# Optimization experiments

Measured on AMD Instinct MI355X. Metric: run time of the kernel, lower is better.

Reference implementation:

```python
import jax, jax.numpy as jnp
import numpy as np
from jax import lax

DT = 0.1


def setup_inputs() -> dict:
    key = jax.random.key(0)
    k1, k2, k3, k4 = jax.random.split(key, 4)
    Bsz, L, D, N, O = 32, 2048, 256, 64, 256
    x = jax.random.normal(k1, (Bsz, L, D), dtype=jnp.float32)
    # Shift A by 3*I so Re(eig(A)) > 0 -> bilinear-discretized A_tilde is stable
    A = jax.random.uniform(k2, (N, N), dtype=jnp.float32) + 3.0 * jnp.eye(N, dtype=jnp.float32)
    B = jax.random.uniform(k3, (N, D), dtype=jnp.float32)
    C = jax.random.uniform(k4, (O, N), dtype=jnp.float32)
    return {"x": x, "A": A, "B": B, "C": C}


def _s4_forward(x, A, B, C):
    N = A.shape[0]
    I = jnp.eye(N, dtype=A.dtype)
    # Bilinear discretization (as written in the torch source)
    tmp_inv = jnp.linalg.inv(I + A * (DT / 2))
    A_tilde = tmp_inv @ (I - A * (DT / 2))          # [N, N]
    B_tilde = (tmp_inv @ B) * DT                    # [N, D]

    L = x.shape[1]

    # K[i] = C @ A_tilde^i @ B_tilde; carry M = A_tilde^i @ B_tilde
    def step(M, _):
        return A_tilde @ M, C @ M                    # emit [O, D]

    _, K = lax.scan(step, B_tilde, None, length=L)   # K: [L, O, D]

    n = 2 * L - 1  # length after torch's F.pad(x, (0,0,0,L-1))
    x_fft = jnp.fft.rfft(x, n=n, axis=1)             # [B, F, D] complex
    K_fft = jnp.fft.rfft(K, n=n, axis=0)             # [F, O, D] complex
    y_fft = jnp.einsum('bfi,foi->bfo', x_fft, K_fft)
    y = jnp.fft.irfft(y_fft, n=n, axis=1)[:, :L]     # [B, L, O]
    return y


def reference(x, A, B, C):
    return _s4_forward(x, A, B, C)
```

## Files before the change

### kernel.cpp

```cpp
#include <hip/hip_runtime.h>

#define B_SZ   32
#define LEN    2048
#define DIM    256
#define NST    64
#define OUTD   256
#define CHUNK  32
#define NCHUNK (LEN / CHUNK)
#define ROWS   (B_SZ * LEN)
#define NCID   (B_SZ * NCHUNK)

#define OFF_AT   0
#define OFF_P32  4096
#define OFF_MINV 8192
#define OFF_CP   12288
#define OFF_S    28672
#define OFF_INST 159744
#define OFF_V    290816
#define WS_FLOATS (OFF_V + (size_t)ROWS * 64)

__device__ __forceinline__ void gload16(const float* gp, float* lds_base,
                                        int lane_off_f) {
#if __has_builtin(__builtin_amdgcn_global_load_lds)
  (void)lane_off_f;
  __builtin_amdgcn_global_load_lds(
      (const __attribute__((address_space(1))) unsigned int*)gp,
      (__attribute__((address_space(3))) unsigned int*)lds_base, 16, 0, 0);
#else
  float4 tmp = *(const float4*)gp;
  *(float4*)(lds_base + lane_off_f) = tmp;
#endif
}

__device__ __forceinline__ void mm64(float* dst, const float* a, const float* b,
                                     int t) {
  const int r0 = 4 * (t >> 4), c0 = 4 * (t & 15);
  float acc[4][4] = {};
  for (int k = 0; k < 64; ++k) {
    float4 bv = *(const float4*)(b + k * 68 + c0);
#pragma unroll
    for (int i = 0; i < 4; ++i) {
      float av = a[(r0 + i) * 68 + k];
      acc[i][0] = fmaf(av, bv.x, acc[i][0]);
      acc[i][1] = fmaf(av, bv.y, acc[i][1]);
      acc[i][2] = fmaf(av, bv.z, acc[i][2]);
      acc[i][3] = fmaf(av, bv.w, acc[i][3]);
    }
  }
  __syncthreads();
#pragma unroll
  for (int i = 0; i < 4; ++i)
    *(float4*)(dst + (r0 + i) * 68 + c0) =
        make_float4(acc[i][0], acc[i][1], acc[i][2], acc[i][3]);
  __syncthreads();
}

__global__ __launch_bounds__(256) void k_fused0(const float* __restrict__ A,
                                                const float* __restrict__ Bm,
                                                const float* __restrict__ Cm,
                                                const float* __restrict__ x,
                                                float* __restrict__ ws) {
  __shared__ __align__(16) float sh[13056];
  const int t = threadIdx.x;

  if (blockIdx.x == 0) {
    float* Pa = sh;
    float* Pb = sh + 4352;
    float* Pc = sh + 8704;
    float* rbM = Pc;
    float* rbI = Pc + 128;
    float* cb  = Pc + 256;

    const int tc = t & 63;
    const int tr = t >> 6;
    float M[16], Iv[16];
#pragma unroll
    for (int i = 0; i < 16; ++i) {
      int r = 16 * tr + i;
      M[i] = 0.05f * A[r * 64 + tc] + (r == tc ? 1.0f : 0.0f);
      Iv[i] = (r == tc) ? 1.0f : 0.0f;
    }
    if (tr == 0) { rbM[tc] = M[0]; rbI[tc] = Iv[0]; }
    if (tc == 0)
      for (int i = 0; i < 16; ++i) cb[16 * tr + i] = M[i];
    __syncthreads();

#pragma unroll
    for (int k = 0; k < 64; ++k) {
      const int cur = (k & 1) * 64, nxt = ((k + 1) & 1) * 64;
      float rinv = 1.0f / rbM[cur + k];
      float rM = rbM[cur + tc] * rinv;
      float rI = rbI[cur + tc] * rinv;
#pragma unroll
      for (int i = 0; i < 16; ++i) {
        int r = 16 * tr + i;
        if (r == k) { M[i] = rM; Iv[i] = rI; }
        else {
          float f = cb[cur + r];
          M[i] = fmaf(-f, rM, M[i]);
          Iv[i] = fmaf(-f, rI, Iv[i]);
        }
      }
      if (k < 63) {
        if (tr == ((k + 1) >> 4)) {
          rbM[nxt + tc] = M[(k + 1) & 15];
          rbI[nxt + tc] = Iv[(k + 1) & 15];
        }
        if (tc == k + 1)
          for (int i = 0; i < 16; ++i) cb[nxt + 16 * tr + i] = M[i];
      }
      __syncthreads();
    }

#pragma unroll
    for (int i = 0; i < 16; ++i) {
      int r = 16 * tr + i;
      float at = 2.0f * Iv[i] - (r == tc ? 1.0f : 0.0f);
      ws[OFF_AT + r * 64 + tc] = at;
      ws[OFF_MINV + r * 64 + tc] = Iv[i];
      Pa[r * 68 + tc] = at;
      Pc[r * 68 + tc] = Iv[i];
    }
    __syncthreads();

    mm64(Pb, Pa, Pa, t);
    mm64(Pa, Pb, Pb, t);
    mm64(Pb, Pa, Pa, t);
    mm64(Pa, Pb, Pb, t);
    mm64(Pb, Pa, Pa, t);
#pragma unroll
    for (int i = 0; i < 16; ++i) {
      int r = 16 * tr + i;
      ws[OFF_P32 + r * 64 + tc] = Pb[r * 68 + tc];
    }

    {
      const float* Crow = Cm + (size_t)t * 64;
      float4 acc4[16];
      for (int q = 0; q < 16; ++q) acc4[q] = make_float4(0.f, 0.f, 0.f, 0.f);
      for (int k = 0; k < 64; k += 4) {
        float4 c4 = *(const float4*)(Crow + k);
        float ck[4] = {c4.x, c4.y, c4.z, c4.w};
#pragma unroll
        for (int kk = 0; kk < 4; ++kk) {
          const float* mrow = Pc + (k + kk) * 68;
          float cc = ck[kk];
#pragma unroll
          for (int q = 0; q < 16; ++q) {
            float4 mv = *(const float4*)(mrow + 4 * q);
            acc4[q].x = fmaf(cc, mv.x, acc4[q].x);
            acc4[q].y = fmaf(cc, mv.y, acc4[q].y);
            acc4[q].z = fmaf(cc, mv.z, acc4[q].z);
            acc4[q].w = fmaf(cc, mv.w, acc4[q].w);
          }
        }
      }
      float* cp = ws + OFF_CP + (size_t)t * 64;
      for (int q = 0; q < 16; ++q)
        *(float4*)(cp + 4 * q) =
            make_float4(0.1f * acc4[q].x, 0.1f * acc4[q].y, 0.1f * acc4[q].z,
                        0.1f * acc4[q].w);
    }
  } else {
    float* xsT = sh;
    float* bsT = sh + 4352;
    const int rowbase = ((int)blockIdx.x - 1) * 64;
    const int r0 = 4 * (t >> 4), m0 = 4 * (t & 15);
    float acc[4][4] = {};
    for (int db = 0; db < 4; ++db) {
      int d0 = db * 64;
      for (int i = 0; i < 4; ++i) {
        int e = 4 * (t + 256 * i);
        int rr = e >> 6, dd = e & 63;
        float4 xv = *(const float4*)(x + (size_t)(rowbase + rr) * 256 + d0 + dd);
        xsT[(dd + 0) * 68 + rr] = xv.x;
        xsT[(dd + 1) * 68 + rr] = xv.y;
        xsT[(dd + 2) * 68 + rr] = xv.z;
        xsT[(dd + 3) * 68 + rr] = xv.w;
        float4 bv = *(const float4*)(Bm + (size_t)rr * 256 + d0 + dd);
        bsT[(dd + 0) * 68 + rr] = bv.x;
        bsT[(dd + 1) * 68 + rr] = bv.y;
        bsT[(dd + 2) * 68 + rr] = bv.z;
        bsT[(dd + 3) * 68 + rr] = bv.w;
      }
      __syncthreads();
      for (int k = 0; k < 64; ++k) {
        float4 av4 = *(const float4*)(xsT + k * 68 + r0);
        float4 bv4 = *(const float4*)(bsT + k * 68 + m0);
        float av[4] = {av4.x, av4.y, av4.z, av4.w};
        float bv[4] = {bv4.x, bv4.y, bv4.z, bv4.w};
        for (int i = 0; i < 4; ++i)
          for (int j = 0; j < 4; ++j) acc[i][j] = fmaf(av[i], bv[j], acc[i][j]);
      }
      __syncthreads();
    }
    float* v = ws + OFF_V;
    for (int i = 0; i < 4; ++i)
      *(float4*)(v + (size_t)(rowbase + r0 + i) * 64 + m0) =
          make_float4(acc[i][0], acc[i][1], acc[i][2], acc[i][3]);
  }
}

__global__ __launch_bounds__(256, 4) void k_chunk(float* __restrict__ ws,
                                                  int phase) {
  __shared__ __align__(16) float Hs[4 * CHUNK * 64];
  __shared__ __align__(16) float hb[4 * 64];
  const int t = threadIdx.x, w = t >> 6, lane = t & 63;
  const int cid = blockIdx.x * 4 + w;
  const int b = cid >> 6, c = cid & (NCHUNK - 1);
  const int r = lane;

  float a[64];
#pragma unroll
  for (int k4 = 0; k4 < 16; ++k4) {
    float4 v4 = *(const float4*)(ws + OFF_AT + r * 64 + 4 * k4);
    a[4 * k4 + 0] = v4.x; a[4 * k4 + 1] = v4.y;
    a[4 * k4 + 2] = v4.z; a[4 * k4 + 3] = v4.w;
  }

  float* Hw = Hs + w * (CHUNK * 64);
  const float* u = ws + OFF_V + (size_t)(b * LEN + c * CHUNK) * 64;
#pragma unroll
  for (int q = 0; q < 8; ++q)
    gload16(u + q * 256 + lane * 4, Hw + q * 256, lane * 4);

  float h0 = (phase == 3)
                 ? ws[OFF_INST + (size_t)(b * NCHUNK + c) * 64 + r]
                 : 0.0f;
  asm volatile("s_waitcnt vmcnt(0)" ::: "memory");
  float* hw = hb + w * 64;
  hw[r] = h0;
  asm volatile("" ::: "memory");

  float* hout = ws + OFF_V + (size_t)(b * LEN + c * CHUNK) * 64;
  float hlast = h0;
#pragma unroll 4
  for (int tt = 0; tt < CHUNK; ++tt) {
    float ac0 = 0.f, ac1 = 0.f, ac2 = 0.f, ac3 = 0.f;
#pragma unroll
    for (int k = 0; k < 64; k += 4) {
      float4 hv = *(const float4*)(hw + k);
      ac0 = fmaf(a[k + 0], hv.x, ac0);
      ac1 = fmaf(a[k + 1], hv.y, ac1);
      ac2 = fmaf(a[k + 2], hv.z, ac2);
      ac3 = fmaf(a[k + 3], hv.w, ac3);
    }
    float hn = ((ac0 + ac1) + (ac2 + ac3)) + Hw[tt * 64 + r];
    hw[r] = hn;
    if (phase == 3) hout[(size_t)tt * 64 + r] = hn;
    hlast = hn;
    asm volatile("" ::: "memory");
  }
  if (phase != 3) ws[OFF_S + (size_t)(b * NCHUNK + c) * 64 + r] = hlast;
}

__global__ __launch_bounds__(256) void k_carry(float* __restrict__ ws) {
  __shared__ __align__(16) float hbc[4][64];
  const int t = threadIdx.x, w = t >> 6, lane = t & 63;
  const int b = blockIdx.x * 4 + w;
  const int r = lane;
  float a[64];
#pragma unroll
  for (int k4 = 0; k4 < 16; ++k4) {
    float4 v4 = *(const float4*)(ws + OFF_P32 + r * 64 + 4 * k4);
    a[4 * k4 + 0] = v4.x; a[4 * k4 + 1] = v4.y;
    a[4 * k4 + 2] = v4.z; a[4 * k4 + 3] = v4.w;
  }
  const float* S = ws + OFF_S + (size_t)b * (NCHUNK * 64);
  float* INST = ws + OFF_INST + (size_t)b * (NCHUNK * 64);
  INST[r] = 0.0f;
  float* hw = hbc[w];
  hw[r] = 0.0f;
  float s_pre = S[r];
  asm volatile("" ::: "memory");
  for (int cc = 1; cc < NCHUNK; ++cc) {
    float s_nxt = (cc < NCHUNK - 1) ? S[(size_t)cc * 64 + r] : 0.0f;
    float ac0 = 0.f, ac1 = 0.f, ac2 = 0.f, ac3 = 0.f;
#pragma unroll
    for (int k = 0; k < 64; k += 4) {
      float4 hv = *(const float4*)(hw + k);
      ac0 = fmaf(a[k + 0], hv.x, ac0);
      ac1 = fmaf(a[k + 1], hv.y, ac1);
      ac2 = fmaf(a[k + 2], hv.z, ac2);
      ac3 = fmaf(a[k + 3], hv.w, ac3);
    }
    float hn = ((ac0 + ac1) + (ac2 + ac3)) + s_pre;
    hw[r] = hn;
    INST[(size_t)cc * 64 + r] = hn;
    s_pre = s_nxt;
    asm volatile("" ::: "memory");
  }
}

__global__ __launch_bounds__(256) void k_ygemm(const float* __restrict__ ws,
                                               float* __restrict__ y) {
  __shared__ __align__(16) float hs[64 * 68];
  __shared__ __align__(16) float cs[64 * 68];
  const int t = threadIdx.x;
  const int rowbase = blockIdx.x * 64;
  const int o0 = blockIdx.y * 64;
  const float* h = ws + OFF_V;
  const float* CP = ws + OFF_CP;
  for (int i = 0; i < 4; ++i) {
    int e = 4 * (t + 256 * i);
    int rr = e >> 6, nn = e & 63;
    *(float4*)(hs + rr * 68 + nn) =
        *(const float4*)(h + (size_t)rowbase * 64 + e);
    float4 cv = *(const float4*)(CP + (size_t)(o0 + rr) * 64 + nn);
    cs[(nn + 0) * 68 + rr] = cv.x;
    cs[(nn + 1) * 68 + rr] = cv.y;
    cs[(nn + 2) * 68 + rr] = cv.z;
    cs[(nn + 3) * 68 + rr] = cv.w;
  }
  __syncthreads();
  const int tr = t >> 4, tc = t & 15;
  const int r0 = tr * 4, c0 = tc * 4;
  float acc[4][4] = {};
  for (int k = 0; k < 64; ++k) {
    float4 cv4 = *(const float4*)(cs + k * 68 + c0);
    float cv[4] = {cv4.x, cv4.y, cv4.z, cv4.w};
    for (int i = 0; i < 4; ++i) {
      float hv = hs[(r0 + i) * 68 + k];
      for (int j = 0; j < 4; ++j) acc[i][j] = fmaf(hv, cv[j], acc[i][j]);
    }
  }
  for (int i = 0; i < 4; ++i)
    *(float4*)(y + (size_t)(rowbase + r0 + i) * 256 + o0 + c0) =
        make_float4(acc[i][0], acc[i][1], acc[i][2], acc[i][3]);
}

extern "C" void kernel_launch(void* const* d_in, const int* in_sizes, int n_in,
                              void* d_out, int out_size, void* d_ws,
                              size_t ws_size, hipStream_t stream) {
  const float* x = (const float*)d_in[0];
  const float* A = (const float*)d_in[1];
  const float* Bm = (const float*)d_in[2];
  const float* Cm = (const float*)d_in[3];
  float* y = (float*)d_out;
  float* ws = (float*)d_ws;
  if (ws_size < (size_t)WS_FLOATS * sizeof(float)) return;

  hipLaunchKernelGGL(k_fused0, dim3(1 + ROWS / 64), dim3(256), 0, stream, A,
                     Bm, Cm, x, ws);
  hipLaunchKernelGGL(k_chunk, dim3(NCID / 4), dim3(256), 0, stream, ws, 1);
  hipLaunchKernelGGL(k_carry, dim3(B_SZ / 4), dim3(256), 0, stream, ws);
  hipLaunchKernelGGL(k_chunk, dim3(NCID / 4), dim3(256), 0, stream, ws, 3);
  hipLaunchKernelGGL(k_ygemm, dim3(ROWS / 64, OUTD / 64), dim3(256), 0, stream,
                     ws, y);
}
```

Measured before the change: 250.2 us.

## Use split-bf16 MFMA for input and output projections, move P32/CP setup into chunk kernel

Rewrites the x·Bᵀ projection and the h·CPᵀ output GEMM to run on bf16 MFMA. Each fp32 operand is split into a high and a low bf16 part, and three MFMAs per tile (hi·hi, lo·hi, hi·lo) recover near-fp32 accuracy. Operands are staged in XOR-swizzled LDS via global_load_lds. The A_tilde^32 power and C·Minv precompute move out of the serial block 0 of k_fused0 into two extra blocks of the first k_chunk launch, shortening the critical path of the first kernel. The split-bf16 scheme trades some precision for matrix-core throughput, and the ygemm grid becomes one block per 64 rows covering all 256 outputs.

```diff
diff --git a/kernel.cpp b/kernel.cpp
--- a/kernel.cpp
+++ b/kernel.cpp
@@ -18,6 +18,10 @@
 #define OFF_INST 159744
 #define OFF_V    290816
 #define WS_FLOATS (OFF_V + (size_t)ROWS * 64)
+
+typedef __attribute__((ext_vector_type(8))) short bf16x8;
+typedef __attribute__((ext_vector_type(4))) float f32x4;
+union U4 { uint4 u; bf16x8 b; };
 
 __device__ __forceinline__ void gload16(const float* gp, float* lds_base,
                                         int lane_off_f) {
@@ -32,6 +36,29 @@
 #endif
 }
 
+__device__ __forceinline__ void split8(float4 a, float4 b, uint4& h, uint4& l) {
+  unsigned int ua0 = __float_as_uint(a.x), ua1 = __float_as_uint(a.y);
+  unsigned int ua2 = __float_as_uint(a.z), ua3 = __float_as_uint(a.w);
+  unsigned int ub0 = __float_as_uint(b.x), ub1 = __float_as_uint(b.y);
+  unsigned int ub2 = __float_as_uint(b.z), ub3 = __float_as_uint(b.w);
+  h.x = (ua0 >> 16) | (ua1 & 0xFFFF0000u);
+  h.y = (ua2 >> 16) | (ua3 & 0xFFFF0000u);
+  h.z = (ub0 >> 16) | (ub1 & 0xFFFF0000u);
+  h.w = (ub2 >> 16) | (ub3 & 0xFFFF0000u);
+  float l0 = a.x - __uint_as_float(ua0 & 0xFFFF0000u);
+  float l1 = a.y - __uint_as_float(ua1 & 0xFFFF0000u);
+  float l2 = a.z - __uint_as_float(ua2 & 0xFFFF0000u);
+  float l3 = a.w - __uint_as_float(ua3 & 0xFFFF0000u);
+  float l4 = b.x - __uint_as_float(ub0 & 0xFFFF0000u);
+  float l5 = b.y - __uint_as_float(ub1 & 0xFFFF0000u);
+  float l6 = b.z - __uint_as_float(ub2 & 0xFFFF0000u);
+  float l7 = b.w - __uint_as_float(ub3 & 0xFFFF0000u);
+  l.x = (__float_as_uint(l0) >> 16) | (__float_as_uint(l1) & 0xFFFF0000u);
+  l.y = (__float_as_uint(l2) >> 16) | (__float_as_uint(l3) & 0xFFFF0000u);
+  l.z = (__float_as_uint(l4) >> 16) | (__float_as_uint(l5) & 0xFFFF0000u);
+  l.w = (__float_as_uint(l6) >> 16) | (__float_as_uint(l7) & 0xFFFF0000u);
+}
+
 __device__ __forceinline__ void mm64(float* dst, const float* a, const float* b,
                                      int t) {
   const int r0 = 4 * (t >> 4), c0 = 4 * (t & 15);
@@ -57,20 +84,15 @@
 
 __global__ __launch_bounds__(256) void k_fused0(const float* __restrict__ A,
                                                 const float* __restrict__ Bm,
-                                                const float* __restrict__ Cm,
                                                 const float* __restrict__ x,
                                                 float* __restrict__ ws) {
-  __shared__ __align__(16) float sh[13056];
+  __shared__ __align__(16) float sh[16384];
   const int t = threadIdx.x;
 
   if (blockIdx.x == 0) {
-    float* Pa = sh;
-    float* Pb = sh + 4352;
-    float* Pc = sh + 8704;
-    float* rbM = Pc;
-    float* rbI = Pc + 128;
-    float* cb  = Pc + 256;
-
+    float* rbM = sh;
+    float* rbI = sh + 128;
+    float* cb  = sh + 256;
     const int tc = t & 63;
     const int tr = t >> 6;
     float M[16], Iv[16];
@@ -84,7 +106,6 @@
     if (tc == 0)
       for (int i = 0; i < 16; ++i) cb[16 * tr + i] = M[i];
     __syncthreads();
-
 #pragma unroll
     for (int k = 0; k < 64; ++k) {
       const int cur = (k & 1) * 64, nxt = ((k + 1) & 1) * 64;
@@ -111,101 +132,136 @@
       }
       __syncthreads();
     }
-
 #pragma unroll
     for (int i = 0; i < 16; ++i) {
       int r = 16 * tr + i;
-      float at = 2.0f * Iv[i] - (r == tc ? 1.0f : 0.0f);
-      ws[OFF_AT + r * 64 + tc] = at;
+      ws[OFF_AT + r * 64 + tc] = 2.0f * Iv[i] - (r == tc ? 1.0f : 0.0f);
       ws[OFF_MINV + r * 64 + tc] = Iv[i];
-      Pa[r * 68 + tc] = at;
-      Pc[r * 68 + tc] = Iv[i];
+    }
+  } else {
+    float* Bl = sh;
+    const int w = t >> 6, lane = t & 63;
+#pragma unroll
+    for (int c2 = 0; c2 < 16; ++c2) {
+      int n = 16 * w + c2;
+      const float* gp = Bm + (size_t)n * 256 + 4 * (lane ^ (n & 7));
+      gload16(gp, Bl + n * 256, lane * 4);
     }
     __syncthreads();
 
-    mm64(Pb, Pa, Pa, t);
-    mm64(Pa, Pb, Pb, t);
-    mm64(Pb, Pa, Pa, t);
-    mm64(Pa, Pb, Pb, t);
-    mm64(Pb, Pa, Pa, t);
-#pragma unroll
-    for (int i = 0; i < 16; ++i) {
-      int r = 16 * tr + i;
-      ws[OFF_P32 + r * 64 + tc] = Pb[r * 68 + tc];
-    }
-
-    {
-      const float* Crow = Cm + (size_t)t * 64;
-      float4 acc4[16];
-      for (int q = 0; q < 16; ++q) acc4[q] = make_float4(0.f, 0.f, 0.f, 0.f);
-      for (int k = 0; k < 64; k += 4) {
-        float4 c4 = *(const float4*)(Crow + k);
-        float ck[4] = {c4.x, c4.y, c4.z, c4.w};
-#pragma unroll
-        for (int kk = 0; kk < 4; ++kk) {
-          const float* mrow = Pc + (k + kk) * 68;
-          float cc = ck[kk];
-#pragma unroll
-          for (int q = 0; q < 16; ++q) {
-            float4 mv = *(const float4*)(mrow + 4 * q);
-            acc4[q].x = fmaf(cc, mv.x, acc4[q].x);
-            acc4[q].y = fmaf(cc, mv.y, acc4[q].y);
-            acc4[q].z = fmaf(cc, mv.z, acc4[q].z);
-            acc4[q].w = fmaf(cc, mv.w, acc4[q].w);
+    const int rowbase = ((int)blockIdx.x - 1) * 64 + 16 * w;
+    const int rr = lane & 15, kb = lane >> 4, key = lane & 7;
+    const float* xp = x + (size_t)(rowbase + rr) * 256 + 8 * kb;
+    f32x4 acc[4] = {{0.f,0.f,0.f,0.f},{0.f,0.f,0.f,0.f},
+                    {0.f,0.f,0.f,0.f},{0.f,0.f,0.f,0.f}};
+    float4 xc0 = *(const float4*)(xp);
+    float4 xc1 = *(const float4*)(xp + 4);
+#pragma unroll
+    for (int ki = 0; ki < 8; ++ki) {
+      float4 xn0, xn1;
+      if (ki < 7) {
+        xn0 = *(const float4*)(xp + 32 * (ki + 1));
+        xn1 = *(const float4*)(xp + 32 * (ki + 1) + 4);
+      }
+      U4 ah, al;
+      split8(xc0, xc1, ah.u, al.u);
+#pragma unroll
+      for (int nt = 0; nt < 4; ++nt) {
+        const float* brow = Bl + (nt * 16 + rr) * 256;
+        int U0 = 8 * ki + 2 * kb;
+        float4 b0 = *(const float4*)(brow + 4 * (U0 ^ key));
+        float4 b1 = *(const float4*)(brow + 4 * ((U0 + 1) ^ key));
+        U4 bh, bl2;
+        split8(b0, b1, bh.u, bl2.u);
+        acc[nt] = __builtin_amdgcn_mfma_f32_16x16x32_bf16(ah.b, bh.b, acc[nt], 0, 0, 0);
+        acc[nt] = __builtin_amdgcn_mfma_f32_16x16x32_bf16(al.b, bh.b, acc[nt], 0, 0, 0);
+        acc[nt] = __builtin_amdgcn_mfma_f32_16x16x32_bf16(ah.b, bl2.b, acc[nt], 0, 0, 0);
+      }
+      if (ki < 7) { xc0 = xn0; xc1 = xn1; }
+    }
+    float* v = ws + OFF_V;
+#pragma unroll
+    for (int nt = 0; nt < 4; ++nt)
+#pragma unroll
+      for (int j = 0; j < 4; ++j)
+        v[(size_t)(rowbase + 4 * kb + j) * 64 + nt * 16 + rr] = acc[nt][j];
+  }
+}
+
+__global__ __launch_bounds__(256, 4) void k_chunk(float* __restrict__ ws,
+                                                  const float* __restrict__ Cm,
+                                                  int phase) {
+  __shared__ __align__(16) float sh[8704];
+  float* Hs = sh;
+  float* hb = sh + 8192;
+  const int t = threadIdx.x, w = t >> 6, lane = t & 63;
+
+  if (blockIdx.x >= NCID / 4) {
+    if (phase != 1) return;
+    if (blockIdx.x == NCID / 4) {
+      float* Pa = sh;
+      float* Pb = sh + 4352;
+#pragma unroll
+      for (int i = 0; i < 4; ++i) {
+        int e = 4 * (t + 256 * i);
+        int r = e >> 6, c2 = e & 63;
+        *(float4*)(Pa + r * 68 + c2) = *(const float4*)(ws + OFF_AT + e);
+      }
+      __syncthreads();
+      mm64(Pb, Pa, Pa, t);
+      mm64(Pa, Pb, Pb, t);
+      mm64(Pb, Pa, Pa, t);
+      mm64(Pa, Pb, Pb, t);
+      mm64(Pb, Pa, Pa, t);
+#pragma unroll
+      for (int i = 0; i < 4; ++i) {
+        int e = 4 * (t + 256 * i);
+        int r = e >> 6, c2 = e & 63;
+        *(float4*)(ws + OFF_P32 + e) = *(const float4*)(Pb + r * 68 + c2);
+      }
+    } else {
+      float* Ms = sh;
+      float* Cs = sh + 4352;
+#pragma unroll
+      for (int i = 0; i < 4; ++i) {
+        int e = 4 * (t + 256 * i);
+        int kk = e >> 6, nn = e & 63;
+        *(float4*)(Ms + kk * 68 + nn) = *(const float4*)(ws + OFF_MINV + e);
+      }
+      __syncthreads();
+      const int r0 = 4 * (t >> 4), c0 = 4 * (t & 15);
+      for (int ob = 0; ob < 4; ++ob) {
+#pragma unroll
+        for (int i = 0; i < 4; ++i) {
+          int e = 4 * (t + 256 * i);
+          int orow = e >> 6, kk = e & 63;
+          *(float4*)(Cs + orow * 68 + kk) =
+              *(const float4*)(Cm + (size_t)(64 * ob + orow) * 64 + kk);
+        }
+        __syncthreads();
+        float acc[4][4] = {};
+        for (int k = 0; k < 64; ++k) {
+          float4 bv = *(const float4*)(Ms + k * 68 + c0);
+#pragma unroll
+          for (int i = 0; i < 4; ++i) {
+            float av = Cs[(r0 + i) * 68 + k];
+            acc[i][0] = fmaf(av, bv.x, acc[i][0]);
+            acc[i][1] = fmaf(av, bv.y, acc[i][1]);
+            acc[i][2] = fmaf(av, bv.z, acc[i][2]);
+            acc[i][3] = fmaf(av, bv.w, acc[i][3]);
           }
         }
-      }
-      float* cp = ws + OFF_CP + (size_t)t * 64;
-      for (int q = 0; q < 16; ++q)
-        *(float4*)(cp + 4 * q) =
-            make_float4(0.1f * acc4[q].x, 0.1f * acc4[q].y, 0.1f * acc4[q].z,
-                        0.1f * acc4[q].w);
-    }
-  } else {
-    float* xsT = sh;
-    float* bsT = sh + 4352;
-    const int rowbase = ((int)blockIdx.x - 1) * 64;
-    const int r0 = 4 * (t >> 4), m0 = 4 * (t & 15);
-    float acc[4][4] = {};
-    for (int db = 0; db < 4; ++db) {
-      int d0 = db * 64;
-      for (int i = 0; i < 4; ++i) {
-        int e = 4 * (t + 256 * i);
-        int rr = e >> 6, dd = e & 63;
-        float4 xv = *(const float4*)(x + (size_t)(rowbase + rr) * 256 + d0 + dd);
-        xsT[(dd + 0) * 68 + rr] = xv.x;
-        xsT[(dd + 1) * 68 + rr] = xv.y;
-        xsT[(dd + 2) * 68 + rr] = xv.z;
-        xsT[(dd + 3) * 68 + rr] = xv.w;
-        float4 bv = *(const float4*)(Bm + (size_t)rr * 256 + d0 + dd);
-        bsT[(dd + 0) * 68 + rr] = bv.x;
-        bsT[(dd + 1) * 68 + rr] = bv.y;
-        bsT[(dd + 2) * 68 + rr] = bv.z;
-        bsT[(dd + 3) * 68 + rr] = bv.w;
-      }
-      __syncthreads();
-      for (int k = 0; k < 64; ++k) {
-        float4 av4 = *(const float4*)(xsT + k * 68 + r0);
-        float4 bv4 = *(const float4*)(bsT + k * 68 + m0);
-        float av[4] = {av4.x, av4.y, av4.z, av4.w};
-        float bv[4] = {bv4.x, bv4.y, bv4.z, bv4.w};
+#pragma unroll
         for (int i = 0; i < 4; ++i)
-          for (int j = 0; j < 4; ++j) acc[i][j] = fmaf(av[i], bv[j], acc[i][j]);
-      }
-      __syncthreads();
-    }
-    float* v = ws + OFF_V;
-    for (int i = 0; i < 4; ++i)
-      *(float4*)(v + (size_t)(rowbase + r0 + i) * 64 + m0) =
-          make_float4(acc[i][0], acc[i][1], acc[i][2], acc[i][3]);
-  }
-}
-
-__global__ __launch_bounds__(256, 4) void k_chunk(float* __restrict__ ws,
-                                                  int phase) {
-  __shared__ __align__(16) float Hs[4 * CHUNK * 64];
-  __shared__ __align__(16) float hb[4 * 64];
-  const int t = threadIdx.x, w = t >> 6, lane = t & 63;
+          *(float4*)(ws + OFF_CP + (size_t)(64 * ob + r0 + i) * 64 + c0) =
+              make_float4(0.1f * acc[i][0], 0.1f * acc[i][1], 0.1f * acc[i][2],
+                          0.1f * acc[i][3]);
+        __syncthreads();
+      }
+    }
+    return;
+  }
+
   const int cid = blockIdx.x * 4 + w;
   const int b = cid >> 6, c = cid & (NCHUNK - 1);
   const int r = lane;
@@ -294,39 +350,56 @@
 
 __global__ __launch_bounds__(256) void k_ygemm(const float* __restrict__ ws,
                                                float* __restrict__ y) {
-  __shared__ __align__(16) float hs[64 * 68];
-  __shared__ __align__(16) float cs[64 * 68];
-  const int t = threadIdx.x;
-  const int rowbase = blockIdx.x * 64;
-  const int o0 = blockIdx.y * 64;
-  const float* h = ws + OFF_V;
-  const float* CP = ws + OFF_CP;
-  for (int i = 0; i < 4; ++i) {
-    int e = 4 * (t + 256 * i);
-    int rr = e >> 6, nn = e & 63;
-    *(float4*)(hs + rr * 68 + nn) =
-        *(const float4*)(h + (size_t)rowbase * 64 + e);
-    float4 cv = *(const float4*)(CP + (size_t)(o0 + rr) * 64 + nn);
-    cs[(nn + 0) * 68 + rr] = cv.x;
-    cs[(nn + 1) * 68 + rr] = cv.y;
-    cs[(nn + 2) * 68 + rr] = cv.z;
-    cs[(nn + 3) * 68 + rr] = cv.w;
+  __shared__ __align__(16) float CPl[256 * 64];
+  const int t = threadIdx.x, w = t >> 6, lane = t & 63;
+#pragma unroll
+  for (int c2 = 0; c2 < 16; ++c2) {
+    int s0 = (w * 16 + c2) * 64;
+    int o = (s0 + lane) >> 4, up = lane & 15;
+    const float* gp = ws + OFF_CP + (size_t)o * 64 + 4 * (up ^ (o & 7));
+    gload16(gp, CPl + s0 * 4, lane * 4);
   }
   __syncthreads();
-  const int tr = t >> 4, tc = t & 15;
-  const int r0 = tr * 4, c0 = tc * 4;
-  float acc[4][4] = {};
-  for (int k = 0; k < 64; ++k) {
-    float4 cv4 = *(const float4*)(cs + k * 68 + c0);
-    float cv[4] = {cv4.x, cv4.y, cv4.z, cv4.w};
-    for (int i = 0; i < 4; ++i) {
-      float hv = hs[(r0 + i) * 68 + k];
-      for (int j = 0; j < 4; ++j) acc[i][j] = fmaf(hv, cv[j], acc[i][j]);
-    }
-  }
-  for (int i = 0; i < 4; ++i)
-    *(float4*)(y + (size_t)(rowbase + r0 + i) * 256 + o0 + c0) =
-        make_float4(acc[i][0], acc[i][1], acc[i][2], acc[i][3]);
+
+  const int rowbase = blockIdx.x * 64 + 16 * w;
+  const int rr = lane & 15, kb = lane >> 4, key = lane & 7;
+  const float* hp = ws + OFF_V + (size_t)(rowbase + rr) * 64 + 8 * kb;
+  float4 h0a = *(const float4*)(hp);
+  float4 h0b = *(const float4*)(hp + 4);
+  float4 h1a = *(const float4*)(hp + 32);
+  float4 h1b = *(const float4*)(hp + 36);
+  U4 ah0, al0, ah1, al1;
+  split8(h0a, h0b, ah0.u, al0.u);
+  split8(h1a, h1b, ah1.u, al1.u);
+
+  f32x4 acc[16];
+#pragma unroll
+  for (int nt = 0; nt < 16; ++nt) acc[nt] = (f32x4){0.f, 0.f, 0.f, 0.f};
+
+#pragma unroll
+  for (int nt = 0; nt < 16; ++nt) {
+    const float* crow = CPl + (nt * 16 + rr) * 64;
+    int U0 = 2 * kb;
+    float4 b0 = *(const float4*)(crow + 4 * (U0 ^ key));
+    float4 b1 = *(const float4*)(crow + 4 * ((U0 + 1) ^ key));
+    U4 bh, bl2;
+    split8(b0, b1, bh.u, bl2.u);
+    acc[nt] = __builtin_amdgcn_mfma_f32_16x16x32_bf16(ah0.b, bh.b, acc[nt], 0, 0, 0);
+    acc[nt] = __builtin_amdgcn_mfma_f32_16x16x32_bf16(al0.b, bh.b, acc[nt], 0, 0, 0);
+    acc[nt] = __builtin_amdgcn_mfma_f32_16x16x32_bf16(ah0.b, bl2.b, acc[nt], 0, 0, 0);
+    U0 = 8 + 2 * kb;
+    b0 = *(const float4*)(crow + 4 * (U0 ^ key));
+    b1 = *(const float4*)(crow + 4 * ((U0 + 1) ^ key));
+    split8(b0, b1, bh.u, bl2.u);
+    acc[nt] = __builtin_amdgcn_mfma_f32_16x16x32_bf16(ah1.b, bh.b, acc[nt], 0, 0, 0);
+    acc[nt] = __builtin_amdgcn_mfma_f32_16x16x32_bf16(al1.b, bh.b, acc[nt], 0, 0, 0);
+    acc[nt] = __builtin_amdgcn_mfma_f32_16x16x32_bf16(ah1.b, bl2.b, acc[nt], 0, 0, 0);
+  }
+#pragma unroll
+  for (int nt = 0; nt < 16; ++nt)
+#pragma unroll
+    for (int j = 0; j < 4; ++j)
+      y[(size_t)(rowbase + 4 * kb + j) * 256 + nt * 16 + rr] = acc[nt][j];
 }
 
 extern "C" void kernel_launch(void* const* d_in, const int* in_sizes, int n_in,
@@ -341,10 +414,9 @@
   if (ws_size < (size_t)WS_FLOATS * sizeof(float)) return;
 
   hipLaunchKernelGGL(k_fused0, dim3(1 + ROWS / 64), dim3(256), 0, stream, A,
-                     Bm, Cm, x, ws);
-  hipLaunchKernelGGL(k_chunk, dim3(NCID / 4), dim3(256), 0, stream, ws, 1);
+                     Bm, x, ws);
+  hipLaunchKernelGGL(k_chunk, dim3(NCID / 4 + 2), dim3(256), 0, stream, ws, Cm, 1);
   hipLaunchKernelGGL(k_carry, dim3(B_SZ / 4), dim3(256), 0, stream, ws);
-  hipLaunchKernelGGL(k_chunk, dim3(NCID / 4), dim3(256), 0, stream, ws, 3);
-  hipLaunchKernelGGL(k_ygemm, dim3(ROWS / 64, OUTD / 64), dim3(256), 0, stream,
-                     ws, y);
-}
+  hipLaunchKernelGGL(k_chunk, dim3(NCID / 4), dim3(256), 0, stream, ws, Cm, 3);
+  hipLaunchKernelGGL(k_ygemm, dim3(ROWS / 64), dim3(256), 0, stream, ws, y);
+}
```

Result: faster. 217.0 us (-13.3%).
